# Optimization experiments

Hardware: AMD Instinct MI355X
Metric: run time of the kernel (lower is better)

## Reference

```python
import math
import jax, jax.numpy as jnp
import numpy as np

B, T, M, S, D, H = 16, 512, 8, 32, 256, 4
HD = D // H


def setup_inputs() -> dict:
    key = jax.random.key(0)
    ks = jax.random.split(key, 16)
    w = 1.0 / math.sqrt(D)
    return {
        'q_temporal': jax.random.normal(ks[0], (B, T, M, D), jnp.float32),
        'q_static': jax.random.normal(ks[1], (B, S, D), jnp.float32),
        'k_temporal': jax.random.normal(ks[2], (B, T, M, D), jnp.float32),
        'v_temporal': jax.random.normal(ks[3], (B, T, M, D), jnp.float32),
        'k_static': jax.random.normal(ks[4], (B, S, D), jnp.float32),
        'v_static': jax.random.normal(ks[5], (B, S, D), jnp.float32),
        'q_w': jax.random.normal(ks[6], (D, D), jnp.float32) * w,
        'q_b': jax.random.normal(ks[7], (D,), jnp.float32) * w,
        'k_w': jax.random.normal(ks[8], (D, D), jnp.float32) * w,
        'k_b': jax.random.normal(ks[9], (D,), jnp.float32) * w,
        'v_w': jax.random.normal(ks[10], (D, D), jnp.float32) * w,
        'v_b': jax.random.normal(ks[11], (D,), jnp.float32) * w,
        'o_w': jax.random.normal(ks[12], (D, D), jnp.float32) * w,
        'o_b': jax.random.normal(ks[13], (D,), jnp.float32) * w,
        'mask_temporal': jax.random.randint(ks[14], (B, T, M), 0, 2).astype(jnp.int32),
        'mask_fcst': jax.random.randint(ks[15], (B, T, M), 0, 2).astype(jnp.int32),
        'mask_static': jnp.ones((B, S), jnp.int32),
    }


def _lin(x, w, b):
    # torch.nn.Linear: y = x @ W^T + b
    return x @ w.T + b


def reference(q_temporal, q_static, k_temporal, v_temporal, k_static, v_static,
              q_w, q_b, k_w, k_b, v_w, v_b, o_w, o_b,
              mask_temporal, mask_fcst, mask_static):
    scale = 1.0 / math.sqrt(HD)

    def heads5(x):  # [B,T,M,D] -> [B,H,T,M,HD]
        return x.reshape(B, T, M, H, HD).transpose(0, 3, 1, 2, 4)

    def heads3(x):  # [B,S,D] -> [B,H,S,HD]
        return x.reshape(B, -1, H, HD).transpose(0, 2, 1, 3)

    Qt = heads5(_lin(q_temporal, q_w, q_b))
    Kt = heads5(_lin(k_temporal, k_w, k_b))
    Vt = heads5(_lin(v_temporal, v_w, v_b))
    Qs = heads3(_lin(q_static, q_w, q_b))
    Ks = heads3(_lin(k_static, k_w, k_b))
    Vs = heads3(_lin(v_static, v_w, v_b))

    # additive masks: 0 where valid (==1), -inf where padded
    mt = jnp.where(mask_temporal == 1, 0.0, -jnp.inf).astype(Qt.dtype)  # [B,T,M]
    ms = jnp.where(mask_static == 1, 0.0, -jnp.inf).astype(Qt.dtype)    # [B,S]

    # ---- temporal query branch ----
    # temp_temp: per-timestep modality-vs-modality attention, column key mask
    Qt_Kt = jnp.einsum('bhtmd,bhtnd->bhtmn', Qt, Kt) * scale + mt[:, None, :, None, :]
    # temp_static: temporal queries vs static keys
    Qt_Ks = jnp.einsum('bhtmd,bhsd->bhtms', Qt, Ks) * scale + ms[:, None, None, None, :]
    tw = jax.nn.softmax(jnp.concatenate([Qt_Kt, Qt_Ks], axis=-1), axis=-1)  # [B,H,T,M,M+S]
    QKV_t = (jnp.einsum('bhtmn,bhtnd->bhtmd', tw[..., :M], Vt)
             + jnp.einsum('bhtms,bhsd->bhtmd', tw[..., M:], Vs))
    out_t = _lin(QKV_t.transpose(0, 2, 3, 1, 4).reshape(B, T, M, D), o_w, o_b)

    # ---- static query branch ----
    Ktf = Kt.reshape(B, H, T * M, HD)  # flatten (T,M) key axis
    Vtf = Vt.reshape(B, H, T * M, HD)
    Qs_Kt = jnp.einsum('bhqd,bhkd->bhqk', Qs, Ktf) * scale + mt.reshape(B, 1, 1, T * M)
    Qs_Ks = jnp.einsum('bhqd,bhsd->bhqs', Qs, Ks) * scale + ms[:, None, None, :]
    sw = jax.nn.softmax(jnp.concatenate([Qs_Kt, Qs_Ks], axis=-1), axis=-1)  # [B,H,S,T*M+S]
    QKV_s = (jnp.einsum('bhqk,bhkd->bhqd', sw[..., :T * M], Vtf)
             + jnp.einsum('bhqs,bhsd->bhqd', sw[..., T * M:], Vs))
    out_s = _lin(QKV_s.transpose(0, 2, 1, 3).reshape(B, S, D), o_w, o_b)

    return (out_t, out_s, tw, sw)
```

## Files before the change

### kernel.cpp

```cpp
#include <hip/hip_runtime.h>

#define B_   16
#define T_   512
#define M_   8
#define S_   32
#define D_   256
#define H_   4
#define HD_  64
#define TM_  4096
#define NKT  40
#define NKS  4128

typedef unsigned short u16;
typedef __attribute__((ext_vector_type(8))) short bf16x8;
typedef __attribute__((ext_vector_type(4))) float f32x4;

__device__ __forceinline__ u16 f2b(float f) {
    union { float f; unsigned u; } v; v.f = f;
    unsigned r = v.u + 0x7FFF + ((v.u >> 16) & 1);
    return (u16)(r >> 16);
}
__device__ __forceinline__ float blo(unsigned u) {
    union { unsigned i; float f; } v; v.i = u << 16; return v.f;
}
__device__ __forceinline__ float bhi(unsigned u) {
    union { unsigned i; float f; } v; v.i = u & 0xFFFF0000u; return v.f;
}
__device__ __forceinline__ float b2f(u16 u) {
    union { unsigned i; float f; } v; v.i = ((unsigned)u) << 16; return v.f;
}
__device__ __forceinline__ unsigned pack2(float lo, float hi) {
    return (unsigned)f2b(lo) | ((unsigned)f2b(hi) << 16);
}
__device__ __forceinline__ uint4 cvt8(float4 a, float4 b) {
    uint4 r;
    r.x = pack2(a.x, a.y); r.y = pack2(a.z, a.w);
    r.z = pack2(b.x, b.y); r.w = pack2(b.z, b.w);
    return r;
}

#define GLL16(g, l) __builtin_amdgcn_global_load_lds( \
    (const __attribute__((address_space(1))) void*)(g), \
    (__attribute__((address_space(3))) void*)(l), 16, 0, 0)

__global__ __launch_bounds__(256) void k_cvt_w(const float* __restrict__ W0,
                                               const float* __restrict__ W1,
                                               const float* __restrict__ W2,
                                               u16* __restrict__ dst)
{
    const int sel = blockIdx.y;
    const float* W = sel == 0 ? W0 : sel == 1 ? W1 : W2;
    u16* d = dst + sel * 65536;
    const int i0 = (blockIdx.x * 256 + threadIdx.x) * 8;
    const float4 a = *(const float4*)(W + i0);
    const float4 b = *(const float4*)(W + i0 + 4);
    *(uint4*)(d + i0) = cvt8(a, b);
}

template<int XBF, int OUTF32>
__device__ __forceinline__ void gemm_body(const void* __restrict__ Xv,
                                          const u16* __restrict__ Wb,
                                          const float* __restrict__ bias,
                                          void* __restrict__ Yv,
                                          int bx, u16* smem)
{
    const int tid = threadIdx.x;
    const size_t r0 = (size_t)bx * 128;
    const int wave = tid >> 6, lane = tid & 63;
    const int c = lane & 15, g = lane >> 4;
    const int swzk = g ^ ((c >> 1) & 3);
    const int swzl = (lane & 3) ^ ((lane >> 3) & 3);
    u16* sA = smem;
    u16* sB = smem + 10240;
    const int ar = tid >> 1, ah = tid & 1;

    f32x4 acc[8][4];
#pragma unroll
    for (int i = 0; i < 8; ++i)
#pragma unroll
        for (int j = 0; j < 4; ++j) acc[i][j] = (f32x4){0, 0, 0, 0};

    float4 fa[2][4];
    uint4  ua[2][2];

#define LOAD_A(k0, s)                                                           \
    if (XBF) {                                                                  \
        const u16* gA = (const u16*)Xv + (r0 + ar) * 256 + (k0) + ah * 16;      \
        ua[s][0] = *(const uint4*)gA; ua[s][1] = *(const uint4*)(gA + 8);       \
    } else {                                                                    \
        const float* gA = (const float*)Xv + (r0 + ar) * 256 + (k0) + ah * 16;  \
        fa[s][0] = *(const float4*)gA;       fa[s][1] = *(const float4*)(gA + 4); \
        fa[s][2] = *(const float4*)(gA + 8); fa[s][3] = *(const float4*)(gA + 12); \
    }
#define WRITE_A(bi, s)                                                          \
    {   u16* d = sA + (bi) * 5120 + ar * 40 + ah * 16;                          \
        if (XBF) { *(uint4*)d = ua[s][0]; *(uint4*)(d + 8) = ua[s][1]; }        \
        else { *(uint4*)d = cvt8(fa[s][0], fa[s][1]);                           \
               *(uint4*)(d + 8) = cvt8(fa[s][2], fa[s][3]); }                   \
    }
#define STAGE_B(k0, bi)                                                         \
    _Pragma("unroll")                                                           \
    for (int i = 0; i < 4; ++i) {                                               \
        const int row = i * 64 + wave * 16 + (lane >> 2);                       \
        GLL16(Wb + (size_t)row * 256 + (k0) + swzl * 8,                         \
              sB + (bi) * 8192 + (i * 256 + wave * 64) * 8);                    \
    }

    {
        STAGE_B(0, 0)
        LOAD_A(0, 0)
        WRITE_A(0, 0)
        LOAD_A(32, 1)
        asm volatile("s_waitcnt lgkmcnt(0)" ::: "memory");
        __builtin_amdgcn_s_barrier();
        __builtin_amdgcn_sched_barrier(0);
    }

#pragma unroll
    for (int k = 0; k < 8; ++k) {
        const int cur = k & 1;
        if (k < 7) { STAGE_B((k + 1) * 32, cur ^ 1) }
        __builtin_amdgcn_sched_barrier(0);
        if (k < 6) { LOAD_A((k + 2) * 32, k & 1) }
        __builtin_amdgcn_sched_barrier(0);

        bf16x8 a[8], b[4];
#pragma unroll
        for (int f = 0; f < 8; ++f)
            a[f] = *(const bf16x8*)(sA + cur * 5120 + (f * 16 + c) * 40 + g * 8);
#pragma unroll
        for (int f = 0; f < 4; ++f)
            b[f] = *(const bf16x8*)(sB + cur * 8192 + (wave * 64 + f * 16 + c) * 32 + swzk * 8);
#pragma unroll
        for (int rf = 0; rf < 8; ++rf)
#pragma unroll
            for (int cf = 0; cf < 4; ++cf)
                acc[rf][cf] = __builtin_amdgcn_mfma_f32_16x16x32_bf16(
                    a[rf], b[cf], acc[rf][cf], 0, 0, 0);
        if (k < 7) WRITE_A(cur ^ 1, (k + 1) & 1)

        if (k <= 5) {
            if (XBF) asm volatile("s_waitcnt vmcnt(2) lgkmcnt(0)" ::: "memory");
            else     asm volatile("s_waitcnt vmcnt(4) lgkmcnt(0)" ::: "memory");
            __builtin_amdgcn_s_barrier();
            __builtin_amdgcn_sched_barrier(0);
        } else if (k == 6) {
            asm volatile("s_waitcnt vmcnt(0) lgkmcnt(0)" ::: "memory");
            __builtin_amdgcn_s_barrier();
            __builtin_amdgcn_sched_barrier(0);
        }
    }
#undef LOAD_A
#undef WRITE_A
#undef STAGE_B

    const int orow = g * 4, ocol = c;
    if (OUTF32) {
#pragma unroll
        for (int cf = 0; cf < 4; ++cf) {
            const int col = wave * 64 + cf * 16 + ocol;
            const float bv = bias[col];
#pragma unroll
            for (int rf = 0; rf < 8; ++rf)
#pragma unroll
                for (int r = 0; r < 4; ++r)
                    ((float*)Yv)[(r0 + rf * 16 + orow + r) * 256 + col] =
                        acc[rf][cf][r] + bv;
        }
    } else {
#pragma unroll
        for (int hh = 0; hh < 2; ++hh) {
            __syncthreads();
#pragma unroll
            for (int cf = 0; cf < 4; ++cf) {
                const int col = wave * 64 + cf * 16 + ocol;
                const float bv = bias[col];
#pragma unroll
                for (int rf4 = 0; rf4 < 4; ++rf4)
#pragma unroll
                    for (int r = 0; r < 4; ++r)
                        smem[(rf4 * 16 + orow + r) * 264 + col] =
                            f2b(acc[hh * 4 + rf4][cf][r] + bv);
            }
            __syncthreads();
#pragma unroll
            for (int i = 0; i < 8; ++i) {
                const int s = i * 256 + tid;
                const int row = s >> 5, seg = s & 31;
                *(uint4*)((u16*)Yv + (r0 + hh * 64 + row) * 256 + seg * 8) =
                    *(const uint4*)(smem + row * 264 + seg * 8);
            }
        }
    }
}

template<int XBF, int OUTF32>
__global__ __launch_bounds__(256, 2) void k_gemm_m(const void* __restrict__ Xv,
                                                   const u16* __restrict__ Wb,
                                                   const float* __restrict__ bias,
                                                   void* __restrict__ Yv)
{
    __shared__ __align__(16) u16 smem[26624];
    gemm_body<XBF, OUTF32>(Xv, Wb, bias, Yv, blockIdx.x, smem);
}

__global__ __launch_bounds__(256, 2) void k_gemm_qkv(
    const float* __restrict__ X0, const float* __restrict__ X1, const float* __restrict__ X2,
    const u16* __restrict__ Wb,
    const float* __restrict__ b0, const float* __restrict__ b1, const float* __restrict__ b2,
    u16* __restrict__ Y0, u16* __restrict__ Y1, u16* __restrict__ Y2)
{
    __shared__ __align__(16) u16 smem[26624];
    const int sel = blockIdx.y;
    const float* X = sel == 0 ? X0 : sel == 1 ? X1 : X2;
    const float* bb = sel == 0 ? b0 : sel == 1 ? b1 : b2;
    u16* Y = sel == 0 ? Y0 : sel == 1 ? Y1 : Y2;
    gemm_body<0, 0>(X, Wb + sel * 65536, bb, Y, blockIdx.x, smem);
}

__global__ __launch_bounds__(256) void k_attn_t(
    const u16* __restrict__ Qt, const u16* __restrict__ Kt, const u16* __restrict__ Vt,
    const u16* __restrict__ Ks, const u16* __restrict__ Vs,
    const int* __restrict__ maskT, const int* __restrict__ maskS,
    float* __restrict__ tw, u16* __restrict__ qkvt)
{
    const int tp = blockIdx.x, b = blockIdx.y;
    const int t0 = tp * 2;
    __shared__ __align__(16) u16 sQ [4 * 2 * 16 * 32];
    __shared__ __align__(16) u16 sKT[4 * 2 * 16 * 32];
    __shared__ __align__(16) u16 sKS[4 * 2 * 32 * 32];
    __shared__ __align__(16) u16 sVT[4 * 64 * 72];
    __shared__ __align__(16) u16 sP [4 * 16 * 72];
    __shared__ int smT[2][8];
    __shared__ int smS[32];
    const int tid = threadIdx.x;

#pragma unroll
    for (int i = 0; i < 2; ++i) {
        const int fl = tid + i * 256;
        const int r = fl >> 5, c32 = fl & 31;
        const int h = c32 >> 3, ks = (c32 >> 2) & 1, seg = c32 & 3;
        const size_t src = (((size_t)b * T_ + t0 + (r >> 3)) * 8 + (r & 7)) * 256 + c32 * 8;
        const int dst = h * 1024 + ks * 512 + r * 32 + seg * 8;
        *(uint4*)(sQ  + dst) = *(const uint4*)(Qt + src);
        *(uint4*)(sKT + dst) = *(const uint4*)(Kt + src);
    }
#pragma unroll
    for (int i = 0; i < 4; ++i) {
        const int fl = tid + i * 256;
        const int r = fl >> 5, c32 = fl & 31;
        const int h = c32 >> 3, ks = (c32 >> 2) & 1, seg = c32 & 3;
        *(uint4*)(sKS + h * 2048 + ks * 1024 + r * 32 + seg * 8) =
            *(const uint4*)(Ks + ((size_t)b * S_ + r) * 256 + c32 * 8);
    }
    {
        const int key = tid & 63, dg = tid >> 6;
        const u16* vrow = nullptr;
        if (key < 16)      vrow = Vt + (((size_t)b * T_ + t0 + (key >> 3)) * 8 + (key & 7)) * 256;
        else if (key < 48) vrow = Vs + ((size_t)b * S_ + (key - 16)) * 256;
#pragma unroll
        for (int i = 0; i < 8; ++i) {
            const int dseg = dg * 8 + i;
            uint4 v = {0, 0, 0, 0};
            if (vrow) v = *(const uint4*)(vrow + dseg * 8);
            const int h = dseg >> 3, dl0 = (dseg & 7) * 8;
            const u16* pv = (const u16*)&v;
#pragma unroll
            for (int j = 0; j < 8; ++j)
                sVT[h * 4608 + (dl0 + j) * 72 + key] = pv[j];
        }
    }
    if (tid < 16) smT[tid >> 3][tid & 7] =
        maskT[((size_t)b * T_ + t0 + (tid >> 3)) * 8 + (tid & 7)];
    if (tid < 32) smS[tid] = maskS[b * S_ + tid];
    __syncthreads();

    const int h = tid >> 6, lane = tid & 63;
    const int c = lane & 15, g = lane >> 4, th = g >> 1;

    f32x4 at = {0,0,0,0}, as0 = {0,0,0,0}, as1 = {0,0,0,0};
#pragma unroll
    for (int ks = 0; ks < 2; ++ks) {
        bf16x8 aq = *(const bf16x8*)(sQ  + h * 1024 + ks * 512 + c * 32 + g * 8);
        bf16x8 bt = *(const bf16x8*)(sKT + h * 1024 + ks * 512 + c * 32 + g * 8);
        bf16x8 b0 = *(const bf16x8*)(sKS + h * 2048 + ks * 1024 + c * 32 + g * 8);
        bf16x8 b1 = *(const bf16x8*)(sKS + h * 2048 + ks * 1024 + 512 + c * 32 + g * 8);
        at  = __builtin_amdgcn_mfma_f32_16x16x32_bf16(aq, bt, at, 0, 0, 0);
        as0 = __builtin_amdgcn_mfma_f32_16x16x32_bf16(aq, b0, as0, 0, 0, 0);
        as1 = __builtin_amdgcn_mfma_f32_16x16x32_bf16(aq, b1, as1, 0, 0, 0);
    }

    const int vt = ((c >> 3) == th) ? smT[th][c & 7] : 0;
    const int v0 = smS[c], v1 = smS[16 + c];
    float st[4], s0[4], s1[4], mx[4];
#pragma unroll
    for (int r = 0; r < 4; ++r) {
        st[r] = vt ? at[r]  * 0.125f : -1e30f;
        s0[r] = v0 ? as0[r] * 0.125f : -1e30f;
        s1[r] = v1 ? as1[r] * 0.125f : -1e30f;
        mx[r] = fmaxf(fmaxf(st[r], s0[r]), s1[r]);
    }
#pragma unroll
    for (int o = 1; o < 16; o <<= 1)
#pragma unroll
        for (int r = 0; r < 4; ++r) mx[r] = fmaxf(mx[r], __shfl_xor(mx[r], o));
    float pt[4], p0[4], p1[4], sum[4];
#pragma unroll
    for (int r = 0; r < 4; ++r) {
        pt[r] = __expf(st[r] - mx[r]);
        p0[r] = __expf(s0[r] - mx[r]);
        p1[r] = __expf(s1[r] - mx[r]);
        sum[r] = pt[r] + p0[r] + p1[r];
    }
#pragma unroll
    for (int o = 1; o < 16; o <<= 1)
#pragma unroll
        for (int r = 0; r < 4; ++r) sum[r] += __shfl_xor(sum[r], o);
#pragma unroll
    for (int r = 0; r < 4; ++r) {
        const float inv = 1.0f / sum[r];
        pt[r] *= inv; p0[r] *= inv; p1[r] *= inv;
    }

#pragma unroll
    for (int r = 0; r < 4; ++r) {
        const int row = g * 4 + r;
        const int tt = t0 + (row >> 3), m = row & 7;
        float* twp = tw + ((((size_t)b * H_ + h) * T_ + tt) * 8 + m) * NKT;
        if ((c >> 3) == th) twp[c & 7] = pt[r];
        twp[8 + c]  = p0[r];
        twp[24 + c] = p1[r];
        u16* sp = sP + h * 1152 + row * 72;
        sp[c]      = f2b(pt[r]);
        sp[16 + c] = f2b(p0[r]);
        sp[32 + c] = f2b(p1[r]);
        sp[48 + c] = 0;
    }

    f32x4 o4[4] = {{0,0,0,0}, {0,0,0,0}, {0,0,0,0}, {0,0,0,0}};
#pragma unroll
    for (int ks = 0; ks < 2; ++ks) {
        bf16x8 pa = *(const bf16x8*)(sP + h * 1152 + c * 72 + ks * 32 + g * 8);
#pragma unroll
        for (int dt = 0; dt < 4; ++dt) {
            bf16x8 pb = *(const bf16x8*)(sVT + h * 4608 + (dt * 16 + c) * 72 + ks * 32 + g * 8);
            o4[dt] = __builtin_amdgcn_mfma_f32_16x16x32_bf16(pa, pb, o4[dt], 0, 0, 0);
        }
    }
#pragma unroll
    for (int dt = 0; dt < 4; ++dt)
#pragma unroll
        for (int r = 0; r < 4; ++r) {
            const int row = g * 4 + r;
            const int tt = t0 + (row >> 3), m = row & 7;
            qkvt[(((size_t)b * T_ + tt) * 8 + m) * 256 + h * 64 + dt * 16 + c] = f2b(o4[dt][r]);
        }
}

__global__ __launch_bounds__(256) void k_attn_s_scores(
    const u16* __restrict__ Qs, const u16* __restrict__ Kt, const u16* __restrict__ Ks,
    const int* __restrict__ maskT, const int* __restrict__ maskS,
    float* __restrict__ raw)
{
    const int ch = blockIdx.x, h = blockIdx.y, b = blockIdx.z;
    const int nk = (ch < 32) ? 128 : 32;
    const int k0 = ch * 128;
    __shared__ __align__(16) u16 sQ[2 * 32 * 32];
    __shared__ __align__(16) u16 sK[2 * 128 * 32];
    __shared__ int sM[128];
    const int tid = threadIdx.x;

    {   const int q = tid >> 3, c8 = tid & 7;
        const int ks = c8 >> 2, seg = c8 & 3;
        *(uint4*)(sQ + ks * 1024 + q * 32 + seg * 8) =
            *(const uint4*)(Qs + ((size_t)b * S_ + q) * 256 + h * 64 + c8 * 8);
    }
#pragma unroll
    for (int i = 0; i < 4; ++i) {
        const int fl = tid + i * 256;
        const int key = fl >> 3, c8 = fl & 7;
        const int ks = c8 >> 2, seg = c8 & 3;
        if (key < nk) {
            const u16* src = (ch < 32)
                ? (Kt + ((size_t)b * TM_ + k0 + key) * 256 + h * 64 + c8 * 8)
                : (Ks + ((size_t)b * S_  +      key) * 256 + h * 64 + c8 * 8);
            *(uint4*)(sK + ks * 4096 + key * 32 + seg * 8) = *(const uint4*)src;
        }
    }
    if (tid < nk) sM[tid] = (ch < 32) ? maskT[(size_t)b * TM_ + k0 + tid]
                                      : maskS[b * S_ + tid];
    __syncthreads();

    const int w = tid >> 6, lane = tid & 63;
    if (w * 32 >= nk) return;
    const int c = lane & 15, g = lane >> 4;

    f32x4 acc[2][2] = {{{0,0,0,0}, {0,0,0,0}}, {{0,0,0,0}, {0,0,0,0}}};
#pragma unroll
    for (int ks = 0; ks < 2; ++ks) {
        bf16x8 a0 = *(const bf16x8*)(sQ + ks * 1024 +        c * 32 + g * 8);
        bf16x8 a1 = *(const bf16x8*)(sQ + ks * 1024 + 512 +  c * 32 + g * 8);
        bf16x8 b0 = *(const bf16x8*)(sK + ks * 4096 + (w * 32 +      c) * 32 + g * 8);
        bf16x8 b1 = *(const bf16x8*)(sK + ks * 4096 + (w * 32 + 16 + c) * 32 + g * 8);
        acc[0][0] = __builtin_amdgcn_mfma_f32_16x16x32_bf16(a0, b0, acc[0][0], 0, 0, 0);
        acc[0][1] = __builtin_amdgcn_mfma_f32_16x16x32_bf16(a0, b1, acc[0][1], 0, 0, 0);
        acc[1][0] = __builtin_amdgcn_mfma_f32_16x16x32_bf16(a1, b0, acc[1][0], 0, 0, 0);
        acc[1][1] = __builtin_amdgcn_mfma_f32_16x16x32_bf16(a1, b1, acc[1][1], 0, 0, 0);
    }
#pragma unroll
    for (int rt = 0; rt < 2; ++rt)
#pragma unroll
        for (int ct = 0; ct < 2; ++ct) {
            const int kl = w * 32 + ct * 16 + c;
            const float madd = sM[kl] ? 0.f : -1e30f;
#pragma unroll
            for (int r = 0; r < 4; ++r) {
                const int q = rt * 16 + g * 4 + r;
                raw[(((size_t)b * H_ + h) * S_ + q) * NKS + k0 + kl] =
                    acc[rt][ct][r] * 0.125f + madd;
            }
        }
}

__global__ __launch_bounds__(256) void k_attn_s_softmax(
    const float* __restrict__ raw, float* __restrict__ sw)
{
    const int q = blockIdx.x, h = blockIdx.y, b = blockIdx.z;
    __shared__ float sRow[NKS];
    __shared__ float red[8];
    const int tid = threadIdx.x;
    const size_t base = (((size_t)b * H_ + h) * S_ + q) * NKS;

    float mx = -1e30f;
    for (int i = tid; i < NKS; i += 256) {
        const float v = raw[base + i];
        sRow[i] = v;
        mx = fmaxf(mx, v);
    }
    for (int o = 32; o; o >>= 1) mx = fmaxf(mx, __shfl_xor(mx, o));
    if ((tid & 63) == 0) red[tid >> 6] = mx;
    __syncthreads();
    mx = fmaxf(fmaxf(red[0], red[1]), fmaxf(red[2], red[3]));

    float sum = 0.f;
    for (int i = tid; i < NKS; i += 256) {
        const float e = __expf(sRow[i] - mx);
        sRow[i] = e;
        sum += e;
    }
    for (int o = 32; o; o >>= 1) sum += __shfl_xor(sum, o);
    if ((tid & 63) == 0) red[4 + (tid >> 6)] = sum;
    __syncthreads();
    sum = (red[4] + red[5]) + (red[6] + red[7]);
    const float inv = 1.0f / sum;

    for (int i = tid; i < NKS; i += 256)
        sw[base + i] = sRow[i] * inv;
}

__global__ __launch_bounds__(256) void k_attn_s_pv_part(
    const float* __restrict__ w, const u16* __restrict__ Vt, const u16* __restrict__ Vs,
    float* __restrict__ part)
{
    const int ch = blockIdx.x, h = blockIdx.y, b = blockIdx.z;
    const int nk = (ch < 32) ? 128 : 32;
    const int k0 = ch * 128;
    __shared__ float sW[32][132];
    __shared__ __align__(16) u16 sV[128 * 64];
    const int tid = threadIdx.x;

#pragma unroll
    for (int i = 0; i < 4; ++i) {
        const int fl = tid + i * 256;
        const int q = fl >> 5, k4 = fl & 31;
        if (k4 * 4 < nk)
            *(float4*)&sW[q][k4 * 4] =
                *(const float4*)(w + (((size_t)b * H_ + h) * S_ + q) * NKS + k0 + k4 * 4);
    }
#pragma unroll
    for (int i = 0; i < 4; ++i) {
        const int fl = tid + i * 256;
        const int key = fl >> 3, pp = fl & 7;
        if (key < nk) {
            const u16* src = (ch < 32)
                ? (Vt + ((size_t)b * TM_ + k0 + key) * D_ + h * HD_ + pp * 8)
                : (Vs + ((size_t)b * S_  +      key) * D_ + h * HD_ + pp * 8);
            ((uint4*)sV)[fl] = *(const uint4*)src;
        }
    }
    __syncthreads();

    const int d = tid & 63, qg = tid >> 6;
    float acc[8] = {0,0,0,0,0,0,0,0};
    for (int kk = 0; kk < nk; kk += 4) {
        const float v0 = b2f(sV[(kk + 0) * 64 + d]);
        const float v1 = b2f(sV[(kk + 1) * 64 + d]);
        const float v2 = b2f(sV[(kk + 2) * 64 + d]);
        const float v3 = b2f(sV[(kk + 3) * 64 + d]);
#pragma unroll
        for (int j = 0; j < 8; ++j) {
            const float4 wv = *(const float4*)&sW[qg * 8 + j][kk];
            acc[j] += wv.x * v0 + wv.y * v1 + wv.z * v2 + wv.w * v3;
        }
    }

    float* pb = part + (((size_t)ch * B_ + b) * H_ + h) * 2048;
#pragma unroll
    for (int j = 0; j < 8; ++j)
        pb[(qg * 8 + j) * 64 + d] = acc[j];
}

__global__ __launch_bounds__(256) void k_attn_s_pv_red(
    const float* __restrict__ part, u16* __restrict__ qkvs)
{
    const int h = blockIdx.x, b = blockIdx.y;
    const int tid = threadIdx.x;
    for (int i = tid; i < 2048; i += 256) {
        float s = 0.f;
#pragma unroll
        for (int c = 0; c < 33; ++c)
            s += part[(((size_t)c * B_ + b) * H_ + h) * 2048 + i];
        const int q = i >> 6, d = i & 63;
        qkvs[((size_t)b * S_ + q) * D_ + h * HD_ + d] = f2b(s);
    }
}

extern "C" void kernel_launch(void* const* d_in, const int* in_sizes, int n_in,
                              void* d_out, int out_size, void* d_ws, size_t ws_size,
                              hipStream_t stream)
{
    const float* q_t = (const float*)d_in[0];
    const float* q_s = (const float*)d_in[1];
    const float* k_t = (const float*)d_in[2];
    const float* v_t = (const float*)d_in[3];
    const float* k_s = (const float*)d_in[4];
    const float* v_s = (const float*)d_in[5];
    const float* q_w = (const float*)d_in[6];
    const float* q_b = (const float*)d_in[7];
    const float* k_w = (const float*)d_in[8];
    const float* k_b = (const float*)d_in[9];
    const float* v_w = (const float*)d_in[10];
    const float* v_b = (const float*)d_in[11];
    const float* o_w = (const float*)d_in[12];
    const float* o_b = (const float*)d_in[13];
    const int* maskT = (const int*)d_in[14];
    const int* maskS = (const int*)d_in[16];
    float* out = (float*)d_out;

    char* ws = (char*)d_ws;
    u16*   Kt   = (u16*)(ws + 0);
    u16*   Vt   = (u16*)(ws + 33554432);
    u16*   QKVt = (u16*)(ws + 67108864);
    float* part = (float*)(ws + 67108864);
    u16*   Wqkv = (u16*)(ws + 67108864);
    u16*   Qs   = (u16*)(ws + 100663296);
    u16*   Ks   = (u16*)(ws + 100925440);
    u16*   Vs   = (u16*)(ws + 101187584);
    u16*   QKVs = (u16*)(ws + 101449728);
    u16*   Qt   = (u16*)(ws + 101711872);
    float* raw  = (float*)(ws + 101711872);
    u16*   Wo   = (u16*)(ws + 101711872);
    if (ws_size < 135528448) return;

    float* out_t = out;
    float* out_s = out + 16777216;
    float* tw    = out + 16908288;
    float* sw    = out + 27394048;

    const dim3 blk(256);
    k_cvt_w<<<dim3(32, 3), blk, 0, stream>>>(q_w, k_w, v_w, Wqkv);

    k_gemm_qkv<<<dim3(512, 3), blk, 0, stream>>>(q_t, k_t, v_t, Wqkv,
                                                 q_b, k_b, v_b, Qt, Kt, Vt);
    k_gemm_qkv<<<dim3(4, 3),   blk, 0, stream>>>(q_s, k_s, v_s, Wqkv,
                                                 q_b, k_b, v_b, Qs, Ks, Vs);

    k_attn_t<<<dim3(256, 16), blk, 0, stream>>>(Qt, Kt, Vt, Ks, Vs, maskT, maskS, tw, QKVt);

    k_cvt_w<<<dim3(32, 1), blk, 0, stream>>>(o_w, o_w, o_w, Wo);
    k_gemm_m<1,1><<<dim3(512), blk, 0, stream>>>(QKVt, Wo, o_b, out_t);

    k_attn_s_scores<<<dim3(33, 4, 16), blk, 0, stream>>>(Qs, Kt, Ks, maskT, maskS, raw);
    k_attn_s_softmax<<<dim3(32, 4, 16), blk, 0, stream>>>(raw, sw);
    k_cvt_w<<<dim3(32, 1), blk, 0, stream>>>(o_w, o_w, o_w, Wo);
    k_attn_s_pv_part<<<dim3(33, 4, 16), blk, 0, stream>>>(sw, Vt, Vs, part);
    k_attn_s_pv_red<<<dim3(4, 16), blk, 0, stream>>>(part, QKVs);

    k_gemm_m<1,1><<<dim3(4),   blk, 0, stream>>>(QKVs, Wo, o_b, out_s);
}
```

Baseline: 261.9 us.

## Add persistent weight-stationary GEMM with full weight in LDS for big projections

Adds a new GEMM kernel that loads the entire 256x256 bf16 weight matrix into shared memory once per block, using an XOR swizzle. Each wave then streams 16-row chunks of the input straight from global memory into MFMA operands, with no A staging in LDS. The kernel replaces the previous tiled GEMMs for the temporal QKV projection and the temporal output projection. This removes repeated weight tile loads and barriers, but needs 128KB of LDS per block, which limits occupancy, and writes outputs with scattered, uncoalesced stores.

```diff
diff --git a/kernel.cpp b/kernel.cpp
--- a/kernel.cpp
+++ b/kernel.cpp
@@ -58,6 +58,85 @@
 }
 
 template<int XBF, int OUTF32>
+__global__ __launch_bounds__(512, 2) void k_gemm_sw(
+    const void* __restrict__ X0, const void* __restrict__ X1, const void* __restrict__ X2,
+    const u16* __restrict__ Wb,
+    const float* __restrict__ b0, const float* __restrict__ b1, const float* __restrict__ b2,
+    void* __restrict__ Y0, void* __restrict__ Y1, void* __restrict__ Y2)
+{
+    __shared__ __align__(16) u16 sW[65536];
+    const int sel = blockIdx.y;
+    const void*  Xv   = sel == 0 ? X0 : sel == 1 ? X1 : X2;
+    const float* bias = sel == 0 ? b0 : sel == 1 ? b1 : b2;
+    void*        Yv   = sel == 0 ? Y0 : sel == 1 ? Y1 : Y2;
+    const u16* W = Wb + sel * 65536;
+    const int tid = threadIdx.x;
+
+#pragma unroll
+    for (int i = 0; i < 16; ++i) {
+        const int s = i * 512 + tid;
+        const int r = s >> 5, blk = s & 31;
+        const uint4 v = *(const uint4*)(W + r * 256 + blk * 8);
+        *(uint4*)(sW + r * 256 + ((blk ^ (r & 7)) * 8)) = v;
+    }
+    __syncthreads();
+
+    const int wave = tid >> 6, lane = tid & 63;
+    const int c = lane & 15, g = lane >> 4;
+
+    float bv[16];
+#pragma unroll
+    for (int ct = 0; ct < 16; ++ct) bv[ct] = bias[ct * 16 + c];
+
+#define LOADA(t, s)                                                             \
+    if (XBF) {                                                                  \
+        ua[s] = *(const uint4*)((const u16*)Xv + (r0 + c) * 256 + (t) * 32 + g * 8); \
+    } else {                                                                    \
+        const float* gA = (const float*)Xv + (r0 + c) * 256 + (t) * 32 + g * 8; \
+        fa[s][0] = *(const float4*)gA; fa[s][1] = *(const float4*)(gA + 4);     \
+    }
+
+    const int nch = gridDim.x * 8;
+    for (int ci = blockIdx.x * 8 + wave; ci < 4096; ci += nch) {
+        const size_t r0 = (size_t)ci * 16;
+        float4 fa[2][2];
+        uint4  ua[2];
+        f32x4 acc[16];
+#pragma unroll
+        for (int ct = 0; ct < 16; ++ct) acc[ct] = (f32x4){0, 0, 0, 0};
+
+        LOADA(0, 0)
+        LOADA(1, 1)
+#pragma unroll
+        for (int t = 0; t < 8; ++t) {
+            uint4 au;
+            if (XBF) au = ua[t & 1];
+            else     au = cvt8(fa[t & 1][0], fa[t & 1][1]);
+            const bf16x8 a = *(const bf16x8*)&au;
+            if (t < 6) LOADA(t + 2, t & 1)
+#pragma unroll
+            for (int ct = 0; ct < 16; ++ct) {
+                const bf16x8 b = *(const bf16x8*)(sW + (ct * 16 + c) * 256
+                                  + (((t * 4 + g) ^ (c & 7)) * 8));
+                acc[ct] = __builtin_amdgcn_mfma_f32_16x16x32_bf16(a, b, acc[ct], 0, 0, 0);
+            }
+        }
+#pragma unroll
+        for (int ct = 0; ct < 16; ++ct) {
+            const int col = ct * 16 + c;
+#pragma unroll
+            for (int r = 0; r < 4; ++r) {
+                const size_t row = r0 + g * 4 + r;
+                const float y = acc[ct][r] + bv[ct];
+                if (OUTF32) ((float*)Yv)[row * 256 + col] = y;
+                else        ((u16*) Yv)[row * 256 + col] = f2b(y);
+            }
+        }
+    }
+#undef LOADA
+}
+
+template<int XBF, int OUTF32>
 __device__ __forceinline__ void gemm_body(const void* __restrict__ Xv,
                                           const u16* __restrict__ Wb,
                                           const float* __restrict__ bias,
@@ -159,13 +238,13 @@
 #pragma unroll
         for (int cf = 0; cf < 4; ++cf) {
             const int col = wave * 64 + cf * 16 + ocol;
-            const float bv = bias[col];
+            const float bvv = bias[col];
 #pragma unroll
             for (int rf = 0; rf < 8; ++rf)
 #pragma unroll
                 for (int r = 0; r < 4; ++r)
                     ((float*)Yv)[(r0 + rf * 16 + orow + r) * 256 + col] =
-                        acc[rf][cf][r] + bv;
+                        acc[rf][cf][r] + bvv;
         }
     } else {
 #pragma unroll
@@ -174,13 +253,13 @@
 #pragma unroll
             for (int cf = 0; cf < 4; ++cf) {
                 const int col = wave * 64 + cf * 16 + ocol;
-                const float bv = bias[col];
+                const float bvv = bias[col];
 #pragma unroll
                 for (int rf4 = 0; rf4 < 4; ++rf4)
 #pragma unroll
                     for (int r = 0; r < 4; ++r)
                         smem[(rf4 * 16 + orow + r) * 264 + col] =
-                            f2b(acc[hh * 4 + rf4][cf][r] + bv);
+                            f2b(acc[hh * 4 + rf4][cf][r] + bvv);
             }
             __syncthreads();
 #pragma unroll
@@ -568,17 +647,19 @@
     float* sw    = out + 27394048;
 
     const dim3 blk(256);
+    const dim3 blk2(512);
     k_cvt_w<<<dim3(32, 3), blk, 0, stream>>>(q_w, k_w, v_w, Wqkv);
 
-    k_gemm_qkv<<<dim3(512, 3), blk, 0, stream>>>(q_t, k_t, v_t, Wqkv,
-                                                 q_b, k_b, v_b, Qt, Kt, Vt);
-    k_gemm_qkv<<<dim3(4, 3),   blk, 0, stream>>>(q_s, k_s, v_s, Wqkv,
-                                                 q_b, k_b, v_b, Qs, Ks, Vs);
+    k_gemm_sw<0, 0><<<dim3(256, 3), blk2, 0, stream>>>(
+        q_t, k_t, v_t, Wqkv, q_b, k_b, v_b, Qt, Kt, Vt);
+    k_gemm_qkv<<<dim3(4, 3), blk, 0, stream>>>(q_s, k_s, v_s, Wqkv,
+                                               q_b, k_b, v_b, Qs, Ks, Vs);
 
     k_attn_t<<<dim3(256, 16), blk, 0, stream>>>(Qt, Kt, Vt, Ks, Vs, maskT, maskS, tw, QKVt);
 
     k_cvt_w<<<dim3(32, 1), blk, 0, stream>>>(o_w, o_w, o_w, Wo);
-    k_gemm_m<1,1><<<dim3(512), blk, 0, stream>>>(QKVt, Wo, o_b, out_t);
+    k_gemm_sw<1, 1><<<dim3(256, 1), blk2, 0, stream>>>(
+        QKVt, QKVt, QKVt, Wo, o_b, o_b, o_b, out_t, out_t, out_t);
 
     k_attn_s_scores<<<dim3(33, 4, 16), blk, 0, stream>>>(Qs, Kt, Ks, maskT, maskS, raw);
     k_attn_s_softmax<<<dim3(32, 4, 16), blk, 0, stream>>>(raw, sw);
@@ -586,5 +667,5 @@
     k_attn_s_pv_part<<<dim3(33, 4, 16), blk, 0, stream>>>(sw, Vt, Vs, part);
     k_attn_s_pv_red<<<dim3(4, 16), blk, 0, stream>>>(part, QKVs);
 
-    k_gemm_m<1,1><<<dim3(4),   blk, 0, stream>>>(QKVs, Wo, o_b, out_s);
-}
+    k_gemm_m<1, 1><<<dim3(4), blk, 0, stream>>>(QKVs, Wo, o_b, out_s);
+}
```

After: 799.0 us. +205.1%, slower.
